# Optimization experiments

Measured on AMD Instinct MI355X. Metric: run time of the kernel, lower is better.

## Reference

```python
import jax, jax.numpy as jnp
from jax import lax
import numpy as np

B, H, W, C = 8, 56, 56, 384
NUM_HEADS, HEAD_CH = 6, 64
BN_EPS = 1e-5
DN = ('NHWC', 'HWIO', 'NHWC')


def conv_proj(x, dw_kernel, bn_scale, bn_bias, bn_mean, bn_var, pw_kernel, stride):
    """Depthwise conv -> BatchNorm (eval) -> 1x1 pointwise conv, all SAME padding."""
    in_ch = x.shape[-1]
    x = lax.conv_general_dilated(x, dw_kernel, (stride, stride), 'SAME',
                                 dimension_numbers=DN, feature_group_count=in_ch)
    x = (x - bn_mean) * (bn_scale / jnp.sqrt(bn_var + BN_EPS)) + bn_bias
    x = lax.conv_general_dilated(x, pw_kernel, (1, 1), 'SAME', dimension_numbers=DN)
    return x


def setup_inputs() -> dict:
    key = jax.random.key(0)
    ks = jax.random.split(key, 16)
    d = {
        'inputs_q': jax.random.normal(ks[0], (B, H, W, C), jnp.float32),
        'inputs_kv': jax.random.normal(ks[1], (B, H, W, C), jnp.float32),
        'out_kernel': jax.random.normal(ks[2], (NUM_HEADS, HEAD_CH, C), jnp.float32) * 0.05,
    }
    for i, p in enumerate(['q', 'k', 'v']):
        d[f'{p}_dw_kernel'] = jax.random.normal(ks[3 + i], (3, 3, 1, C), jnp.float32) * 0.1
        d[f'{p}_bn_scale'] = jnp.ones((C,), jnp.float32)
        d[f'{p}_bn_bias'] = jnp.zeros((C,), jnp.float32)
        d[f'{p}_bn_mean'] = jnp.zeros((C,), jnp.float32)
        d[f'{p}_bn_var'] = jnp.ones((C,), jnp.float32)
        d[f'{p}_pw_kernel'] = jax.random.normal(ks[6 + i], (1, 1, C, NUM_HEADS * HEAD_CH), jnp.float32) * 0.05
    return d


def reference(inputs_q, inputs_kv,
              q_dw_kernel, q_bn_scale, q_bn_bias, q_bn_mean, q_bn_var, q_pw_kernel,
              k_dw_kernel, k_bn_scale, k_bn_bias, k_bn_mean, k_bn_var, k_pw_kernel,
              v_dw_kernel, v_bn_scale, v_bn_bias, v_bn_mean, v_bn_var, v_pw_kernel,
              out_kernel):
    q = conv_proj(inputs_q, q_dw_kernel, q_bn_scale, q_bn_bias, q_bn_mean, q_bn_var, q_pw_kernel, 1)
    k = conv_proj(inputs_kv, k_dw_kernel, k_bn_scale, k_bn_bias, k_bn_mean, k_bn_var, k_pw_kernel, 2)
    v = conv_proj(inputs_kv, v_dw_kernel, v_bn_scale, v_bn_bias, v_bn_mean, v_bn_var, v_pw_kernel, 2)

    def to_tokens(x):  # [b,H,W,h*d] -> [b,HW,h,d]
        b, hh, ww, _ = x.shape
        return x.reshape(b, hh * ww, NUM_HEADS, HEAD_CH)

    q = to_tokens(q) / jnp.sqrt(jnp.float32(HEAD_CH))
    k = to_tokens(k)
    v = to_tokens(v)

    attn = jnp.einsum('bqhd,bkhd->bhqk', q, k)       # [b,h,Nq,Nkv]
    attn = jax.nn.softmax(attn, axis=-1)
    out = jnp.einsum('bhqk,bkhd->bqhd', attn, v)     # [b,Nq,h,d]
    out = jnp.einsum('bqhd,hdo->bqo', out, out_kernel)  # DenseGeneral over (h,d)
    return out
```

## Files before the change

kernel.cpp:

```cpp
#include <hip/hip_runtime.h>
#include <hip/hip_bf16.h>
#include <hip/hip_fp16.h>

#define BB 8
#define HH 56
#define WW 56
#define CC 384
#define NHD 6
#define DD 64
#define HK 28
#define WK 28
#define NQ (HH*WW)
#define NKV (HK*WK)
#define NTOK (BB*NQ)
#define NTOKKV (BB*NKV)
#define BN_EPS 1e-5f
#define LOG2E 1.44269504f

typedef _Float16 f16;
typedef _Float16 f16x2 __attribute__((ext_vector_type(2)));
typedef _Float16 f16x4 __attribute__((ext_vector_type(4)));
typedef _Float16 f16x8 __attribute__((ext_vector_type(8)));
typedef float f32x4 __attribute__((ext_vector_type(4)));

__device__ __forceinline__ float fast_exp2(float x) {
#if __has_builtin(__builtin_amdgcn_exp2f)
  return __builtin_amdgcn_exp2f(x);
#else
  return __expf(x * 0.69314718056f);
#endif
}

__device__ __forceinline__ f16x4 pack4(float p0, float p1, float p2, float p3) {
#if __has_builtin(__builtin_amdgcn_cvt_pkrtz)
  f16x2 a = __builtin_bit_cast(f16x2, __builtin_amdgcn_cvt_pkrtz(p0, p1));
  f16x2 b = __builtin_bit_cast(f16x2, __builtin_amdgcn_cvt_pkrtz(p2, p3));
  return __builtin_shufflevector(a, b, 0, 1, 2, 3);
#else
  f16x4 r; r[0] = (f16)p0; r[1] = (f16)p1; r[2] = (f16)p2; r[3] = (f16)p3;
  return r;
#endif
}

__device__ __forceinline__ void dw_s1_body(
    int blk, int tid, const float* __restrict__ in, const float* __restrict__ w,
    const float* __restrict__ bns, const float* __restrict__ bnb,
    const float* __restrict__ bnm, const float* __restrict__ bnv,
    f16* __restrict__ out) {
  int idx = blk * 256 + tid;
  int pp = idx / 96;
  int c = (idx % 96) * 4;
  int b = pp / 784;
  int rem = pp % 784;
  int yh = rem / 28, xh = rem % 28;
  int y0 = yh * 2, x0 = xh * 2;
  const float4 z4 = {0.f, 0.f, 0.f, 0.f};

  float4 V[4][4];
#pragma unroll
  for (int ry = 0; ry < 4; ++ry) {
    const int iy = y0 - 1 + ry;
    const bool vy = (unsigned)iy < (unsigned)HH;
    const float* rp = in + ((size_t)(b * HH + (vy ? iy : 0)) * WW) * CC + c;
    V[ry][0] = (vy && x0 > 0)      ? *(const float4*)(rp + (size_t)(x0 - 1) * CC) : z4;
    V[ry][1] = vy                  ? *(const float4*)(rp + (size_t)x0 * CC)       : z4;
    V[ry][2] = vy                  ? *(const float4*)(rp + (size_t)(x0 + 1) * CC) : z4;
    V[ry][3] = (vy && x0 < WW - 2) ? *(const float4*)(rp + (size_t)(x0 + 2) * CC) : z4;
  }
  float4 W[9];
#pragma unroll
  for (int i = 0; i < 9; ++i) W[i] = *(const float4*)(w + i * CC + c);

  const float4 s = *(const float4*)(bns + c);
  const float4 bi = *(const float4*)(bnb + c);
  const float4 m = *(const float4*)(bnm + c);
  const float4 va = *(const float4*)(bnv + c);
  const float gx = s.x * rsqrtf(va.x + BN_EPS);
  const float gy = s.y * rsqrtf(va.y + BN_EPS);
  const float gz = s.z * rsqrtf(va.z + BN_EPS);
  const float gw = s.w * rsqrtf(va.w + BN_EPS);

#pragma unroll
  for (int dy = 0; dy < 2; ++dy)
#pragma unroll
    for (int dx = 0; dx < 2; ++dx) {
      float ax = 0.f, ay = 0.f, az = 0.f, aw = 0.f;
#pragma unroll
      for (int ky = 0; ky < 3; ++ky)
#pragma unroll
        for (int kx = 0; kx < 3; ++kx) {
          const float4 v = V[dy + ky][dx + kx];
          const float4 wk = W[ky * 3 + kx];
          ax = fmaf(v.x, wk.x, ax); ay = fmaf(v.y, wk.y, ay);
          az = fmaf(v.z, wk.z, az); aw = fmaf(v.w, wk.w, aw);
        }
      f16x4 r;
      r[0] = (f16)fmaf(ax - m.x, gx, bi.x);
      r[1] = (f16)fmaf(ay - m.y, gy, bi.y);
      r[2] = (f16)fmaf(az - m.z, gz, bi.z);
      r[3] = (f16)fmaf(aw - m.w, gw, bi.w);
      const size_t pix = (size_t)b * NQ + (size_t)(y0 + dy) * WW + (x0 + dx);
      *(f16x4*)(out + pix * CC + c) = r;
    }
}

__device__ __forceinline__ void dw_s2_body(
    int blk, int tid, const float* __restrict__ in,
    const float* __restrict__ wk_, const float* __restrict__ kbs, const float* __restrict__ kbb,
    const float* __restrict__ kbm, const float* __restrict__ kbv,
    const float* __restrict__ wv_, const float* __restrict__ vbs, const float* __restrict__ vbb,
    const float* __restrict__ vbm, const float* __restrict__ vbv,
    f16* __restrict__ outk, f16* __restrict__ outv) {
  int idx = blk * 256 + tid;
  int pp = idx / 96;
  int c = (idx % 96) * 4;
  int b = pp / 392;
  int rem = pp % 392;
  int oy = rem / 14, xh = rem % 14;
  int ox0 = xh * 2;
  int iy0 = oy * 2, ix0 = ox0 * 2;
  const float4 z4 = {0.f, 0.f, 0.f, 0.f};

  float4 V[3][5];
#pragma unroll
  for (int ry = 0; ry < 3; ++ry) {
    const int iy = iy0 + ry;
    const bool vy = iy < HH;
    const float* rp = in + ((size_t)(b * HH + (vy ? iy : 0)) * WW) * CC + c;
#pragma unroll
    for (int cx = 0; cx < 5; ++cx) {
      const int ix = ix0 + cx;
      V[ry][cx] = (vy && ix < WW) ? *(const float4*)(rp + (size_t)ix * CC) : z4;
    }
  }

  {
    float4 W[9];
#pragma unroll
    for (int i = 0; i < 9; ++i) W[i] = *(const float4*)(wk_ + i * CC + c);
    const float4 s = *(const float4*)(kbs + c);
    const float4 bi = *(const float4*)(kbb + c);
    const float4 m = *(const float4*)(kbm + c);
    const float4 va = *(const float4*)(kbv + c);
    const float gx = s.x * rsqrtf(va.x + BN_EPS);
    const float gy = s.y * rsqrtf(va.y + BN_EPS);
    const float gz = s.z * rsqrtf(va.z + BN_EPS);
    const float gw = s.w * rsqrtf(va.w + BN_EPS);
#pragma unroll
    for (int dx = 0; dx < 2; ++dx) {
      float ax = 0.f, ay = 0.f, az = 0.f, aw = 0.f;
#pragma unroll
      for (int ky = 0; ky < 3; ++ky)
#pragma unroll
        for (int kx = 0; kx < 3; ++kx) {
          const float4 v = V[ky][2 * dx + kx];
          const float4 wk = W[ky * 3 + kx];
          ax = fmaf(v.x, wk.x, ax); ay = fmaf(v.y, wk.y, ay);
          az = fmaf(v.z, wk.z, az); aw = fmaf(v.w, wk.w, aw);
        }
      f16x4 r;
      r[0] = (f16)fmaf(ax - m.x, gx, bi.x);
      r[1] = (f16)fmaf(ay - m.y, gy, bi.y);
      r[2] = (f16)fmaf(az - m.z, gz, bi.z);
      r[3] = (f16)fmaf(aw - m.w, gw, bi.w);
      const size_t pix = (size_t)b * NKV + (size_t)oy * WK + (ox0 + dx);
      *(f16x4*)(outk + pix * CC + c) = r;
    }
  }
  {
    float4 W[9];
#pragma unroll
    for (int i = 0; i < 9; ++i) W[i] = *(const float4*)(wv_ + i * CC + c);
    const float4 s = *(const float4*)(vbs + c);
    const float4 bi = *(const float4*)(vbb + c);
    const float4 m = *(const float4*)(vbm + c);
    const float4 va = *(const float4*)(vbv + c);
    const float gx = s.x * rsqrtf(va.x + BN_EPS);
    const float gy = s.y * rsqrtf(va.y + BN_EPS);
    const float gz = s.z * rsqrtf(va.z + BN_EPS);
    const float gw = s.w * rsqrtf(va.w + BN_EPS);
#pragma unroll
    for (int dx = 0; dx < 2; ++dx) {
      float ax = 0.f, ay = 0.f, az = 0.f, aw = 0.f;
#pragma unroll
      for (int ky = 0; ky < 3; ++ky)
#pragma unroll
        for (int kx = 0; kx < 3; ++kx) {
          const float4 v = V[ky][2 * dx + kx];
          const float4 wk = W[ky * 3 + kx];
          ax = fmaf(v.x, wk.x, ax); ay = fmaf(v.y, wk.y, ay);
          az = fmaf(v.z, wk.z, az); aw = fmaf(v.w, wk.w, aw);
        }
      f16x4 r;
      r[0] = (f16)fmaf(ax - m.x, gx, bi.x);
      r[1] = (f16)fmaf(ay - m.y, gy, bi.y);
      r[2] = (f16)fmaf(az - m.z, gz, bi.z);
      r[3] = (f16)fmaf(aw - m.w, gw, bi.w);
      const size_t pix = (size_t)b * NKV + (size_t)oy * WK + (ox0 + dx);
      *(f16x4*)(outv + pix * CC + c) = r;
    }
  }
}

__global__ __launch_bounds__(256) void preprocess(
    const float* __restrict__ inputs_q, const float* __restrict__ inputs_kv,
    const float* __restrict__ q_dwk, const float* __restrict__ q_bs,
    const float* __restrict__ q_bb, const float* __restrict__ q_bm,
    const float* __restrict__ q_bv,
    const float* __restrict__ k_dwk, const float* __restrict__ k_bs,
    const float* __restrict__ k_bb, const float* __restrict__ k_bm,
    const float* __restrict__ k_bv,
    const float* __restrict__ v_dwk, const float* __restrict__ v_bs,
    const float* __restrict__ v_bb, const float* __restrict__ v_bm,
    const float* __restrict__ v_bv,
    const float* __restrict__ w0, const float* __restrict__ w1,
    const float* __restrict__ w2, const float* __restrict__ w3,
    f16* __restrict__ o0, f16* __restrict__ o1,
    f16* __restrict__ o2, f16* __restrict__ o3,
    f16* __restrict__ qdw, f16* __restrict__ kdw, f16* __restrict__ vdw) {
  __shared__ float t[32][33];
  const int bid = blockIdx.x;
  const int tid = threadIdx.x;
  if (bid < 2352) {
    const int lb = (bid & 7) * 294 + (bid >> 3);
    dw_s1_body(lb, tid, inputs_q, q_dwk, q_bs, q_bb, q_bm, q_bv, qdw);
  } else if (bid < 3528) {
    const int r = bid - 2352;
    const int lb = (r & 7) * 147 + (r >> 3);
    dw_s2_body(lb, tid, inputs_kv,
               k_dwk, k_bs, k_bb, k_bm, k_bv,
               v_dwk, v_bs, v_bb, v_bm, v_bv, kdw, vdw);
  } else {
    const int r = bid - 3528;
    const int z = r / 144, rem = r % 144;
    const int bx = rem % 12, by = rem / 12;
    const float* src = z == 0 ? w0 : z == 1 ? w1 : z == 2 ? w2 : w3;
    f16* dst = z == 0 ? o0 : z == 1 ? o1 : z == 2 ? o2 : o3;
    const int k0 = bx * 32, n0 = by * 32;
    const int x = tid & 31, y = tid >> 5;
#pragma unroll
    for (int i = 0; i < 4; ++i) t[y + i * 8][x] = src[(size_t)(k0 + y + i * 8) * 384 + n0 + x];
    __syncthreads();
#pragma unroll
    for (int i = 0; i < 4; ++i)
      dst[(size_t)(n0 + y + i * 8) * 384 + k0 + x] = (f16)t[x][y + i * 8];
  }
}

template <int MODE>
__device__ __forceinline__ void gemm_body(
    const f16* __restrict__ A, const f16* __restrict__ Bt,
    float* __restrict__ Cf, f16* __restrict__ Ch, float scale,
    int row0, int col0) {
  __shared__ f16 As[128 * 64];
  __shared__ f16 Bs[128 * 64];
  const int tid = threadIdx.x;
  const int wave = tid >> 6, lane = tid & 63;
  const int c = lane & 15, g = lane >> 4;
  const int wr = wave >> 1, wc = wave & 1;

  const int s_base = wave * 64 + lane;
  f32x4 acc[4][4] = {};

  for (int k0 = 0; k0 < 384; k0 += 64) {
    __syncthreads();
#pragma unroll
    for (int j = 0; j < 4; ++j) {
      const int s = j * 256 + s_base;
      const int row = s >> 3, sch = s & 7;
      const int lch = sch ^ (row & 7);
      const f16* sa = A + (size_t)(row0 + row) * 384 + k0 + lch * 8;
      __builtin_amdgcn_global_load_lds(
          (const __attribute__((address_space(1))) void*)sa,
          (__attribute__((address_space(3))) void*)(As + j * 2048 + wave * 512), 16, 0, 0);
      const f16* sb = Bt + (size_t)(col0 + row) * 384 + k0 + lch * 8;
      __builtin_amdgcn_global_load_lds(
          (const __attribute__((address_space(1))) void*)sb,
          (__attribute__((address_space(3))) void*)(Bs + j * 2048 + wave * 512), 16, 0, 0);
    }
    __syncthreads();

#pragma unroll
    for (int kh = 0; kh < 2; ++kh) {
      f16x8 bf[4];
#pragma unroll
      for (int n = 0; n < 4; ++n) {
        const int row = wc * 64 + n * 16 + c;
        bf[n] = *(const f16x8*)(Bs + (size_t)row * 64 + ((kh * 4 + g) ^ (row & 7)) * 8);
      }
#pragma unroll
      for (int m = 0; m < 4; ++m) {
        const int row = wr * 64 + m * 16 + c;
        f16x8 af = *(const f16x8*)(As + (size_t)row * 64 + ((kh * 4 + g) ^ (row & 7)) * 8);
#pragma unroll
        for (int n = 0; n < 4; ++n)
          acc[m][n] = __builtin_amdgcn_mfma_f32_16x16x32_f16(af, bf[n], acc[m][n], 0, 0, 0);
      }
    }
  }

  if (MODE == 2) {
#pragma unroll
    for (int m = 0; m < 4; ++m)
#pragma unroll
      for (int n = 0; n < 4; ++n) {
        const int gr = row0 + wr * 64 + m * 16 + g * 4;
        const int col = col0 + wc * 64 + n * 16 + c;
        const int bb = gr / NKV;
        const int kv = gr - bb * NKV;
        f16x4 pk;
#pragma unroll
        for (int r = 0; r < 4; ++r) pk[r] = (f16)(acc[m][n][r] * scale);
        *(f16x4*)(Ch + ((size_t)bb * 384 + col) * NKV + kv) = pk;
      }
  } else {
#pragma unroll
    for (int m = 0; m < 4; ++m)
#pragma unroll
      for (int n = 0; n < 4; ++n)
#pragma unroll
        for (int r = 0; r < 4; ++r) {
          const size_t row = row0 + wr * 64 + m * 16 + g * 4 + r;
          const size_t col = col0 + wc * 64 + n * 16 + c;
          if (MODE == 1) Ch[row * 384 + col] = (f16)(acc[m][n][r] * scale);
          else           Cf[row * 384 + col] = acc[m][n][r] * scale;
        }
  }
}

__global__ __launch_bounds__(256) void gemm_qkv(
    const f16* __restrict__ qdw, const f16* __restrict__ wqt, f16* __restrict__ qf, float qscale,
    const f16* __restrict__ kdw, const f16* __restrict__ wkt, f16* __restrict__ kf,
    const f16* __restrict__ vdw, const f16* __restrict__ wvt, f16* __restrict__ vtp) {
  const int blk = blockIdx.x;
  if (blk < 588) {
    gemm_body<1>(qdw, wqt, nullptr, qf, qscale, (blk % 196) * 128, (blk / 196) * 128);
  } else if (blk < 735) {
    const int r = blk - 588;
    gemm_body<1>(kdw, wkt, nullptr, kf, 1.0f, (r % 49) * 128, (r / 49) * 128);
  } else {
    const int r = blk - 735;
    gemm_body<2>(vdw, wvt, nullptr, vtp, 1.0f, (r % 49) * 128, (r / 49) * 128);
  }
}

template <int MODE>
__global__ __launch_bounds__(256) void gemm_mfma(
    const f16* __restrict__ A, const f16* __restrict__ Bt,
    float* __restrict__ Cf, f16* __restrict__ Ch, float scale) {
  gemm_body<MODE>(A, Bt, Cf, Ch, scale, blockIdx.x * 128, blockIdx.y * 128);
}

__global__ __launch_bounds__(256) void attn_mfma(
    const f16* __restrict__ qp, const f16* __restrict__ kp,
    const f16* __restrict__ vt, f16* __restrict__ op) {
  __shared__ f16 Ks[2][64 * 64];
  __shared__ f16 Vs[2][64 * 64];
  __shared__ f16 Ps[4][16 * 64];
  const int bid0 = blockIdx.x;
  const int lb = (bid0 & 7) * 294 + (bid0 >> 3);
  const int qt = lb % 49;
  const int bh = lb / 49;
  const int h = bh % NHD, b = bh / NHD;
  const int tid = threadIdx.x;
  const int wave = tid >> 6, lane = tid & 63;
  const int c = lane & 15, g = lane >> 4;

  const size_t qrow = (size_t)b * NQ + qt * 64 + wave * 16 + c;
  f16x8 qa[2];
  qa[0] = *(const f16x8*)(qp + qrow * 384 + h * 64 + g * 8);
  qa[1] = *(const f16x8*)(qp + qrow * 384 + h * 64 + 32 + g * 8);

  f16x8 vones;
#pragma unroll
  for (int j = 0; j < 8; ++j) vones[j] = (f16)1.0f;

  const int tid8 = tid >> 3, tch = tid & 7;
  const int lch = tch ^ (tid8 & 7);

  const f16* kbase = kp + ((size_t)b * NKV) * 384 + h * 64;
  const f16* vbase = vt + ((size_t)(b * 384 + h * 64)) * NKV;

  float mrun = -1e30f;
  f32x4 o[4] = {};
  f32x4 osum = {};
  f16* prow = &Ps[wave][0];

  f16x8 kr0, kr1, vr0, vr1;
  kr0 = *(const f16x8*)(kbase + (size_t)tid8 * 384 + lch * 8);
  kr1 = *(const f16x8*)(kbase + (size_t)(32 + tid8) * 384 + lch * 8);
  vr0 = *(const f16x8*)(vbase + (size_t)tid8 * NKV + lch * 8);
  vr1 = *(const f16x8*)(vbase + (size_t)(32 + tid8) * NKV + lch * 8);

  int cur = 0;
  for (int ti = 0; ti < 13; ++ti) {
    f16* ksw = &Ks[cur][0];
    f16* vsw = &Vs[cur][0];
    *(f16x8*)(ksw + tid * 8) = kr0;
    *(f16x8*)(ksw + 2048 + tid * 8) = kr1;
    *(f16x8*)(vsw + tid * 8) = vr0;
    *(f16x8*)(vsw + 2048 + tid * 8) = vr1;
    if (ti + 1 < 13) {
      const int t0n = (ti + 1) * 64;
      int kvA = t0n + tid8;        if (kvA > NKV - 1) kvA = NKV - 1;
      int kvB = t0n + 32 + tid8;   if (kvB > NKV - 1) kvB = NKV - 1;
      int colc = t0n + lch * 8;    if (colc > NKV - 8) colc = NKV - 8;
      kr0 = *(const f16x8*)(kbase + (size_t)kvA * 384 + lch * 8);
      kr1 = *(const f16x8*)(kbase + (size_t)kvB * 384 + lch * 8);
      vr0 = *(const f16x8*)(vbase + (size_t)tid8 * NKV + colc);
      vr1 = *(const f16x8*)(vbase + (size_t)(32 + tid8) * NKV + colc);
    }
    __syncthreads();
    const f16* ksb = &Ks[cur][0];
    const f16* vsb = &Vs[cur][0];

    if (ti < 12) {
      f32x4 s[4] = {};
      __builtin_amdgcn_s_setprio(1);
#pragma unroll
      for (int kh = 0; kh < 2; ++kh) {
#pragma unroll
        for (int ct = 0; ct < 4; ++ct) {
          const int row = ct * 16 + c;
          const int sch = (kh * 4 + g) ^ (row & 7);
          f16x8 kb = *(const f16x8*)(ksb + row * 64 + sch * 8);
          s[ct] = __builtin_amdgcn_mfma_f32_16x16x32_f16(kb, qa[kh], s[ct], 0, 0, 0);
        }
      }
      __builtin_amdgcn_s_setprio(0);

      float mt = s[0][0];
#pragma unroll
      for (int ct = 0; ct < 4; ++ct)
#pragma unroll
        for (int r = 0; r < 4; ++r) mt = fmaxf(mt, s[ct][r]);
      mt = fmaxf(mt, __shfl_xor(mt, 16));
      mt = fmaxf(mt, __shfl_xor(mt, 32));

      if (__ballot(mt > mrun + 8.0f)) {
        const float mnew = fmaxf(mrun, mt);
        const float corr = fast_exp2(mrun - mnew);
        mrun = mnew;
#pragma unroll
        for (int r = 0; r < 4; ++r) {
          const float co = __shfl(corr, g * 4 + r);
#pragma unroll
          for (int dt = 0; dt < 4; ++dt) o[dt][r] *= co;
          osum[r] *= co;
        }
      }

#pragma unroll
      for (int ct = 0; ct < 4; ++ct) {
        const float p0 = fast_exp2(s[ct][0] - mrun);
        const float p1 = fast_exp2(s[ct][1] - mrun);
        const float p2 = fast_exp2(s[ct][2] - mrun);
        const float p3 = fast_exp2(s[ct][3] - mrun);
        const int sch = (ct * 2 + (g >> 1)) ^ (c & 7);
        *(f16x4*)(prow + c * 64 + sch * 8 + (g & 1) * 4) = pack4(p0, p1, p2, p3);
      }

      __builtin_amdgcn_s_setprio(1);
#pragma unroll
      for (int ks = 0; ks < 2; ++ks) {
        const int sp = (ks * 4 + g) ^ (c & 7);
        f16x8 pa = *(const f16x8*)(prow + c * 64 + sp * 8);
#pragma unroll
        for (int dt = 0; dt < 4; ++dt) {
          const int d = dt * 16 + c;
          f16x8 vb = *(const f16x8*)(vsb + d * 64 + sp * 8);
          o[dt] = __builtin_amdgcn_mfma_f32_16x16x32_f16(pa, vb, o[dt], 0, 0, 0);
        }
        osum = __builtin_amdgcn_mfma_f32_16x16x32_f16(pa, vones, osum, 0, 0, 0);
      }
      __builtin_amdgcn_s_setprio(0);
    } else {
      f32x4 s0 = {};
      __builtin_amdgcn_s_setprio(1);
#pragma unroll
      for (int kh = 0; kh < 2; ++kh) {
        const int sch = (kh * 4 + g) ^ (c & 7);
        f16x8 kb = *(const f16x8*)(ksb + c * 64 + sch * 8);
        s0 = __builtin_amdgcn_mfma_f32_16x16x32_f16(kb, qa[kh], s0, 0, 0, 0);
      }
      __builtin_amdgcn_s_setprio(0);

      float mt = fmaxf(fmaxf(s0[0], s0[1]), fmaxf(s0[2], s0[3]));
      mt = fmaxf(mt, __shfl_xor(mt, 16));
      mt = fmaxf(mt, __shfl_xor(mt, 32));
      if (__ballot(mt > mrun + 8.0f)) {
        const float mnew = fmaxf(mrun, mt);
        const float corr = fast_exp2(mrun - mnew);
        mrun = mnew;
#pragma unroll
        for (int r = 0; r < 4; ++r) {
          const float co = __shfl(corr, g * 4 + r);
#pragma unroll
          for (int dt = 0; dt < 4; ++dt) o[dt][r] *= co;
          osum[r] *= co;
        }
      }

      {
        const float p0 = fast_exp2(s0[0] - mrun);
        const float p1 = fast_exp2(s0[1] - mrun);
        const float p2 = fast_exp2(s0[2] - mrun);
        const float p3 = fast_exp2(s0[3] - mrun);
        const int sch0 = (0 + (g >> 1)) ^ (c & 7);
        *(f16x4*)(prow + c * 64 + sch0 * 8 + (g & 1) * 4) = pack4(p0, p1, p2, p3);
        const int sch1 = (2 + (g >> 1)) ^ (c & 7);
        f16x4 z = {};
        *(f16x4*)(prow + c * 64 + sch1 * 8 + (g & 1) * 4) = z;
      }

      __builtin_amdgcn_s_setprio(1);
      {
        const int sp = g ^ (c & 7);
        f16x8 pa = *(const f16x8*)(prow + c * 64 + sp * 8);
#pragma unroll
        for (int dt = 0; dt < 4; ++dt) {
          const int d = dt * 16 + c;
          f16x8 vb = *(const f16x8*)(vsb + d * 64 + sp * 8);
          o[dt] = __builtin_amdgcn_mfma_f32_16x16x32_f16(pa, vb, o[dt], 0, 0, 0);
        }
        osum = __builtin_amdgcn_mfma_f32_16x16x32_f16(pa, vones, osum, 0, 0, 0);
      }
      __builtin_amdgcn_s_setprio(0);
    }
    cur ^= 1;
  }

  f16* obase = op + ((size_t)(b * NQ + qt * 64 + wave * 16)) * 384 + h * 64;
#pragma unroll
  for (int r = 0; r < 4; ++r) {
    const float iv = 1.0f / osum[r];
#pragma unroll
    for (int dt = 0; dt < 4; ++dt)
      obase[(size_t)(g * 4 + r) * 384 + dt * 16 + c] = (f16)(o[dt][r] * iv);
  }
}

extern "C" void kernel_launch(void* const* d_in, const int* in_sizes, int n_in,
                              void* d_out, int out_size, void* d_ws, size_t ws_size,
                              hipStream_t stream) {
  const float* inputs_q  = (const float*)d_in[0];
  const float* inputs_kv = (const float*)d_in[1];
  const float* out_kern  = (const float*)d_in[2];
  const float* q_dwk = (const float*)d_in[3];
  const float* q_bs  = (const float*)d_in[4];
  const float* q_bb  = (const float*)d_in[5];
  const float* q_bm  = (const float*)d_in[6];
  const float* q_bv  = (const float*)d_in[7];
  const float* q_pwk = (const float*)d_in[8];
  const float* k_dwk = (const float*)d_in[9];
  const float* k_bs  = (const float*)d_in[10];
  const float* k_bb  = (const float*)d_in[11];
  const float* k_bm  = (const float*)d_in[12];
  const float* k_bv  = (const float*)d_in[13];
  const float* k_pwk = (const float*)d_in[14];
  const float* v_dwk = (const float*)d_in[15];
  const float* v_bs  = (const float*)d_in[16];
  const float* v_bb  = (const float*)d_in[17];
  const float* v_bm  = (const float*)d_in[18];
  const float* v_bv  = (const float*)d_in[19];
  const float* v_pwk = (const float*)d_in[20];

  char* wsb = (char*)d_ws;
  f16* qdw = (f16*)(wsb + 0);
  f16* kdw = (f16*)(wsb + 19267584);
  f16* vdw = (f16*)(wsb + 24084480);
  f16* qf  = (f16*)(wsb + 28901376);
  f16* kf  = (f16*)(wsb + 48168960);
  f16* vtp = (f16*)(wsb + 57802752);
  f16* of  = (f16*)(wsb + 62619648);
  f16* wqt = (f16*)(wsb + 81887232);
  f16* wkt = (f16*)(wsb + 82182144);
  f16* wvt = (f16*)(wsb + 82477056);
  f16* wot = (f16*)(wsb + 82771968);

  preprocess<<<4104, 256, 0, stream>>>(
      inputs_q, inputs_kv,
      q_dwk, q_bs, q_bb, q_bm, q_bv,
      k_dwk, k_bs, k_bb, k_bm, k_bv,
      v_dwk, v_bs, v_bb, v_bm, v_bv,
      q_pwk, k_pwk, v_pwk, out_kern, wqt, wkt, wvt, wot,
      qdw, kdw, vdw);
  gemm_qkv<<<882, 256, 0, stream>>>(qdw, wqt, qf, 0.125f * LOG2E,
                                    kdw, wkt, kf, vdw, wvt, vtp);
  attn_mfma<<<BB * NHD * 49, 256, 0, stream>>>(qf, kf, vtp, of);
  gemm_mfma<0><<<dim3(196, 3), 256, 0, stream>>>(of, wot, (float*)d_out, nullptr, 1.0f);
}
```

Before: 136.1 us.

## Software-pipeline attention loop: compute next QK scores while softmaxing current tile

Restructures the flash-attention inner loop so the QK^T MFMAs for tile i+1 are issued after the PV MFMAs of tile i, and the global prefetch is moved two tiles ahead with a prologue that stages the first tile. This lets the exp/softmax VALU work of one tile overlap with matrix work of the next and hides more global load latency. In exchange it adds a second __syncthreads per iteration, carries extra score registers (snext), and may raise register pressure and lower occupancy.

```diff
diff --git a/kernel.cpp b/kernel.cpp
--- a/kernel.cpp
+++ b/kernel.cpp
@@ -391,17 +391,43 @@
   kr1 = *(const f16x8*)(kbase + (size_t)(32 + tid8) * 384 + lch * 8);
   vr0 = *(const f16x8*)(vbase + (size_t)tid8 * NKV + lch * 8);
   vr1 = *(const f16x8*)(vbase + (size_t)(32 + tid8) * NKV + lch * 8);
+  *(f16x8*)(&Ks[0][0] + tid * 8) = kr0;
+  *(f16x8*)(&Ks[0][0] + 2048 + tid * 8) = kr1;
+  *(f16x8*)(&Vs[0][0] + tid * 8) = vr0;
+  *(f16x8*)(&Vs[0][0] + 2048 + tid * 8) = vr1;
+  kr0 = *(const f16x8*)(kbase + (size_t)(64 + tid8) * 384 + lch * 8);
+  kr1 = *(const f16x8*)(kbase + (size_t)(96 + tid8) * 384 + lch * 8);
+  vr0 = *(const f16x8*)(vbase + (size_t)tid8 * NKV + 64 + lch * 8);
+  vr1 = *(const f16x8*)(vbase + (size_t)(32 + tid8) * NKV + 64 + lch * 8);
+  __syncthreads();
+
+  f32x4 scur[4] = {};
+  __builtin_amdgcn_s_setprio(1);
+#pragma unroll
+  for (int kh = 0; kh < 2; ++kh) {
+#pragma unroll
+    for (int ct = 0; ct < 4; ++ct) {
+      const int row = ct * 16 + c;
+      const int sch = (kh * 4 + g) ^ (row & 7);
+      f16x8 kb = *(const f16x8*)(&Ks[0][0] + row * 64 + sch * 8);
+      scur[ct] = __builtin_amdgcn_mfma_f32_16x16x32_f16(kb, qa[kh], scur[ct], 0, 0, 0);
+    }
+  }
+  __builtin_amdgcn_s_setprio(0);
 
   int cur = 0;
   for (int ti = 0; ti < 13; ++ti) {
-    f16* ksw = &Ks[cur][0];
-    f16* vsw = &Vs[cur][0];
-    *(f16x8*)(ksw + tid * 8) = kr0;
-    *(f16x8*)(ksw + 2048 + tid * 8) = kr1;
-    *(f16x8*)(vsw + tid * 8) = vr0;
-    *(f16x8*)(vsw + 2048 + tid * 8) = vr1;
+    const int nxt = cur ^ 1;
     if (ti + 1 < 13) {
-      const int t0n = (ti + 1) * 64;
+      f16* ksw = &Ks[nxt][0];
+      f16* vsw = &Vs[nxt][0];
+      *(f16x8*)(ksw + tid * 8) = kr0;
+      *(f16x8*)(ksw + 2048 + tid * 8) = kr1;
+      *(f16x8*)(vsw + tid * 8) = vr0;
+      *(f16x8*)(vsw + 2048 + tid * 8) = vr1;
+    }
+    if (ti + 2 < 13) {
+      const int t0n = (ti + 2) * 64;
       int kvA = t0n + tid8;        if (kvA > NKV - 1) kvA = NKV - 1;
       int kvB = t0n + 32 + tid8;   if (kvB > NKV - 1) kvB = NKV - 1;
       int colc = t0n + lch * 8;    if (colc > NKV - 8) colc = NKV - 8;
@@ -410,82 +436,12 @@
       vr0 = *(const f16x8*)(vbase + (size_t)tid8 * NKV + colc);
       vr1 = *(const f16x8*)(vbase + (size_t)(32 + tid8) * NKV + colc);
     }
-    __syncthreads();
-    const f16* ksb = &Ks[cur][0];
-    const f16* vsb = &Vs[cur][0];
-
     if (ti < 12) {
-      f32x4 s[4] = {};
-      __builtin_amdgcn_s_setprio(1);
-#pragma unroll
-      for (int kh = 0; kh < 2; ++kh) {
-#pragma unroll
-        for (int ct = 0; ct < 4; ++ct) {
-          const int row = ct * 16 + c;
-          const int sch = (kh * 4 + g) ^ (row & 7);
-          f16x8 kb = *(const f16x8*)(ksb + row * 64 + sch * 8);
-          s[ct] = __builtin_amdgcn_mfma_f32_16x16x32_f16(kb, qa[kh], s[ct], 0, 0, 0);
-        }
-      }
-      __builtin_amdgcn_s_setprio(0);
-
-      float mt = s[0][0];
+      float mt = scur[0][0];
 #pragma unroll
       for (int ct = 0; ct < 4; ++ct)
 #pragma unroll
-        for (int r = 0; r < 4; ++r) mt = fmaxf(mt, s[ct][r]);
-      mt = fmaxf(mt, __shfl_xor(mt, 16));
-      mt = fmaxf(mt, __shfl_xor(mt, 32));
-
-      if (__ballot(mt > mrun + 8.0f)) {
-        const float mnew = fmaxf(mrun, mt);
-        const float corr = fast_exp2(mrun - mnew);
-        mrun = mnew;
-#pragma unroll
-        for (int r = 0; r < 4; ++r) {
-          const float co = __shfl(corr, g * 4 + r);
-#pragma unroll
-          for (int dt = 0; dt < 4; ++dt) o[dt][r] *= co;
-          osum[r] *= co;
-        }
-      }
-
-#pragma unroll
-      for (int ct = 0; ct < 4; ++ct) {
-        const float p0 = fast_exp2(s[ct][0] - mrun);
-        const float p1 = fast_exp2(s[ct][1] - mrun);
-        const float p2 = fast_exp2(s[ct][2] - mrun);
-        const float p3 = fast_exp2(s[ct][3] - mrun);
-        const int sch = (ct * 2 + (g >> 1)) ^ (c & 7);
-        *(f16x4*)(prow + c * 64 + sch * 8 + (g & 1) * 4) = pack4(p0, p1, p2, p3);
-      }
-
-      __builtin_amdgcn_s_setprio(1);
-#pragma unroll
-      for (int ks = 0; ks < 2; ++ks) {
-        const int sp = (ks * 4 + g) ^ (c & 7);
-        f16x8 pa = *(const f16x8*)(prow + c * 64 + sp * 8);
-#pragma unroll
-        for (int dt = 0; dt < 4; ++dt) {
-          const int d = dt * 16 + c;
-          f16x8 vb = *(const f16x8*)(vsb + d * 64 + sp * 8);
-          o[dt] = __builtin_amdgcn_mfma_f32_16x16x32_f16(pa, vb, o[dt], 0, 0, 0);
-        }
-        osum = __builtin_amdgcn_mfma_f32_16x16x32_f16(pa, vones, osum, 0, 0, 0);
-      }
-      __builtin_amdgcn_s_setprio(0);
-    } else {
-      f32x4 s0 = {};
-      __builtin_amdgcn_s_setprio(1);
-#pragma unroll
-      for (int kh = 0; kh < 2; ++kh) {
-        const int sch = (kh * 4 + g) ^ (c & 7);
-        f16x8 kb = *(const f16x8*)(ksb + c * 64 + sch * 8);
-        s0 = __builtin_amdgcn_mfma_f32_16x16x32_f16(kb, qa[kh], s0, 0, 0, 0);
-      }
-      __builtin_amdgcn_s_setprio(0);
-
-      float mt = fmaxf(fmaxf(s0[0], s0[1]), fmaxf(s0[2], s0[3]));
+        for (int r = 0; r < 4; ++r) mt = fmaxf(mt, scur[ct][r]);
       mt = fmaxf(mt, __shfl_xor(mt, 16));
       mt = fmaxf(mt, __shfl_xor(mt, 32));
       if (__ballot(mt > mrun + 8.0f)) {
@@ -500,22 +456,50 @@
           osum[r] *= co;
         }
       }
-
-      {
-        const float p0 = fast_exp2(s0[0] - mrun);
-        const float p1 = fast_exp2(s0[1] - mrun);
-        const float p2 = fast_exp2(s0[2] - mrun);
-        const float p3 = fast_exp2(s0[3] - mrun);
-        const int sch0 = (0 + (g >> 1)) ^ (c & 7);
-        *(f16x4*)(prow + c * 64 + sch0 * 8 + (g & 1) * 4) = pack4(p0, p1, p2, p3);
-        const int sch1 = (2 + (g >> 1)) ^ (c & 7);
-        f16x4 z = {};
-        *(f16x4*)(prow + c * 64 + sch1 * 8 + (g & 1) * 4) = z;
-      }
-
-      __builtin_amdgcn_s_setprio(1);
-      {
-        const int sp = g ^ (c & 7);
+#pragma unroll
+      for (int ct = 0; ct < 4; ++ct) {
+        const float p0 = fast_exp2(scur[ct][0] - mrun);
+        const float p1 = fast_exp2(scur[ct][1] - mrun);
+        const float p2 = fast_exp2(scur[ct][2] - mrun);
+        const float p3 = fast_exp2(scur[ct][3] - mrun);
+        const int sch = (ct * 2 + (g >> 1)) ^ (c & 7);
+        *(f16x4*)(prow + c * 64 + sch * 8 + (g & 1) * 4) = pack4(p0, p1, p2, p3);
+      }
+    } else {
+      float mt = fmaxf(fmaxf(scur[0][0], scur[0][1]), fmaxf(scur[0][2], scur[0][3]));
+      mt = fmaxf(mt, __shfl_xor(mt, 16));
+      mt = fmaxf(mt, __shfl_xor(mt, 32));
+      if (__ballot(mt > mrun + 8.0f)) {
+        const float mnew = fmaxf(mrun, mt);
+        const float corr = fast_exp2(mrun - mnew);
+        mrun = mnew;
+#pragma unroll
+        for (int r = 0; r < 4; ++r) {
+          const float co = __shfl(corr, g * 4 + r);
+#pragma unroll
+          for (int dt = 0; dt < 4; ++dt) o[dt][r] *= co;
+          osum[r] *= co;
+        }
+      }
+      const float p0 = fast_exp2(scur[0][0] - mrun);
+      const float p1 = fast_exp2(scur[0][1] - mrun);
+      const float p2 = fast_exp2(scur[0][2] - mrun);
+      const float p3 = fast_exp2(scur[0][3] - mrun);
+      const int sch0 = (0 + (g >> 1)) ^ (c & 7);
+      *(f16x4*)(prow + c * 64 + sch0 * 8 + (g & 1) * 4) = pack4(p0, p1, p2, p3);
+      const int sch1 = (2 + (g >> 1)) ^ (c & 7);
+      f16x4 z = {};
+      *(f16x4*)(prow + c * 64 + sch1 * 8 + (g & 1) * 4) = z;
+    }
+    __syncthreads();
+    const f16* vsb = &Vs[cur][0];
+    const f16* ksb = &Ks[nxt][0];
+
+    __builtin_amdgcn_s_setprio(1);
+    if (ti < 12) {
+#pragma unroll
+      for (int ks = 0; ks < 2; ++ks) {
+        const int sp = (ks * 4 + g) ^ (c & 7);
         f16x8 pa = *(const f16x8*)(prow + c * 64 + sp * 8);
 #pragma unroll
         for (int dt = 0; dt < 4; ++dt) {
@@ -525,9 +509,43 @@
         }
         osum = __builtin_amdgcn_mfma_f32_16x16x32_f16(pa, vones, osum, 0, 0, 0);
       }
-      __builtin_amdgcn_s_setprio(0);
-    }
-    cur ^= 1;
+    } else {
+      const int sp = g ^ (c & 7);
+      f16x8 pa = *(const f16x8*)(prow + c * 64 + sp * 8);
+#pragma unroll
+      for (int dt = 0; dt < 4; ++dt) {
+        const int d = dt * 16 + c;
+        f16x8 vb = *(const f16x8*)(vsb + d * 64 + sp * 8);
+        o[dt] = __builtin_amdgcn_mfma_f32_16x16x32_f16(pa, vb, o[dt], 0, 0, 0);
+      }
+      osum = __builtin_amdgcn_mfma_f32_16x16x32_f16(pa, vones, osum, 0, 0, 0);
+    }
+
+    f32x4 snext[4] = {};
+    if (ti + 1 < 12) {
+#pragma unroll
+      for (int kh = 0; kh < 2; ++kh) {
+#pragma unroll
+        for (int ct = 0; ct < 4; ++ct) {
+          const int row = ct * 16 + c;
+          const int sch = (kh * 4 + g) ^ (row & 7);
+          f16x8 kb = *(const f16x8*)(ksb + row * 64 + sch * 8);
+          snext[ct] = __builtin_amdgcn_mfma_f32_16x16x32_f16(kb, qa[kh], snext[ct], 0, 0, 0);
+        }
+      }
+    } else if (ti + 1 == 12) {
+#pragma unroll
+      for (int kh = 0; kh < 2; ++kh) {
+        const int sch = (kh * 4 + g) ^ (c & 7);
+        f16x8 kb = *(const f16x8*)(ksb + c * 64 + sch * 8);
+        snext[0] = __builtin_amdgcn_mfma_f32_16x16x32_f16(kb, qa[kh], snext[0], 0, 0, 0);
+      }
+    }
+    __builtin_amdgcn_s_setprio(0);
+    __syncthreads();
+#pragma unroll
+    for (int i = 0; i < 4; ++i) scur[i] = snext[i];
+    cur = nxt;
   }
 
   f16* obase = op + ((size_t)(b * NQ + qt * 64 + wave * 16)) * 384 + h * 64;
```

After: 140.9 us. +3.5%, slower.
